# Performance work log

Hardware: AMD Instinct MI355X
Metric: run time of the kernel (lower is better)

Reference implementation:

```python
import jax, jax.numpy as jnp
import numpy as np

N_SRC = 50000
N_DST = 50000
N_EDGE = 600000
HID = 128
NUM_R = 6  # num_ratings + 1 weight matrices


def setup_inputs() -> dict:
    key = jax.random.key(0)
    ks = jax.random.split(key, 8)
    return {
        "src_features": jax.random.normal(ks[0], (N_SRC, HID), dtype=jnp.float32),
        "dst_features": jax.random.normal(ks[1], (N_DST, HID), dtype=jnp.float32),
        "W_r": jax.random.normal(ks[2], (NUM_R, HID, HID), dtype=jnp.float32),
        "W_lin": jax.random.normal(ks[3], (HID, 2 * HID), dtype=jnp.float32) / np.sqrt(2.0 * HID),
        "b_lin": jax.random.normal(ks[4], (HID,), dtype=jnp.float32) * 0.01,
        "edge_src": jax.random.randint(ks[5], (N_EDGE,), 0, N_SRC, dtype=jnp.int32),
        "edge_dst": jax.random.randint(ks[6], (N_EDGE,), 0, N_DST, dtype=jnp.int32),
        "rating": jax.random.randint(ks[7], (N_EDGE,), 0, NUM_R, dtype=jnp.int32),
    }


def reference(src_features, dst_features, W_r, W_lin, b_lin, edge_src, edge_dst, rating):
    # Gather source features per edge: [E, H]
    h_src = src_features[edge_src]
    # Per-edge rating-indexed matvec m_e = W_r[rating_e] @ h_src_e.
    # Avoid materializing [E, H, H] gathered weights: loop over the small
    # fixed set of rating matrices and mask-accumulate dense GEMMs.
    num_r = W_r.shape[0]
    m = jnp.zeros_like(h_src)
    for r in range(num_r):
        m = m + jnp.where((rating == r)[:, None], h_src @ W_r[r].T, jnp.zeros((), h_src.dtype))
    # Mean aggregation into destination nodes (0 for isolated nodes, like DGL).
    num_dst = dst_features.shape[0]
    sums = jax.ops.segment_sum(m, edge_dst, num_segments=num_dst)
    counts = jax.ops.segment_sum(jnp.ones((m.shape[0],), m.dtype), edge_dst, num_segments=num_dst)
    h_neigh = sums / jnp.maximum(counts, 1.0)[:, None]
    # concat + linear + relu
    h_cat = jnp.concatenate([dst_features, h_neigh], axis=1)  # [N_dst, 2H]
    return jax.nn.relu(h_cat @ W_lin.T + b_lin)
```

## Files before the change

kernel.cpp:

```cpp
#include <hip/hip_runtime.h>

#define HID 128
#define BM 64
#define BN 128
#define BKS 32
#define ALD (BKS + 8)
#define SCAN_BLK 256
#define SCAN_ELEMS 1024

typedef float v4f __attribute__((ext_vector_type(4)));
typedef short v8s __attribute__((ext_vector_type(8)));

__device__ __forceinline__ void split_bf16(float v, unsigned short& hi, unsigned short& lo) {
  const unsigned int u = __float_as_uint(v);
  hi = (unsigned short)(u >> 16);
  const float rem = v - __uint_as_float(u & 0xffff0000u);
  lo = (unsigned short)(__float_as_uint(rem) >> 16);
}

__global__ void compose_Bt(const float* __restrict__ W_lin, const float* __restrict__ W_r,
                           unsigned short* __restrict__ Bth, unsigned short* __restrict__ Btl,
                           int KT) {
  const int k = blockIdx.x;
  const int n = threadIdx.x;
  float v;
  if (k < HID) {
    v = W_lin[n * (2 * HID) + k];
  } else {
    const int rr = (k - HID) >> 7;
    const int j  = (k - HID) & (HID - 1);
    const float* wl = W_lin + n * (2 * HID) + HID;
    const float* wr = W_r + (size_t)rr * HID * HID + j;
    float acc = 0.f;
#pragma unroll 8
    for (int i2 = 0; i2 < HID; ++i2)
      acc = fmaf(wl[i2], wr[i2 * HID], acc);
    v = acc;
  }
  unsigned short hi, lo;
  split_bf16(v, hi, lo);
  Bth[(size_t)n * KT + k] = hi;
  Btl[(size_t)n * KT + k] = lo;
}

__global__ void hist_kernel(const int* __restrict__ ed, const int* __restrict__ er,
                            int* __restrict__ hist, int NE, int NUMR) {
  const int i = blockIdx.x * blockDim.x + threadIdx.x;
  if (i < NE) atomicAdd(hist + ed[i] * NUMR + er[i], 1);
}

__global__ __launch_bounds__(SCAN_BLK)
void scan_phaseA(const int* __restrict__ cnt, int* __restrict__ partials, int n) {
  __shared__ int red[SCAN_BLK];
  const int tid = threadIdx.x;
  const int base = blockIdx.x * SCAN_ELEMS + tid * 4;
  int s = 0;
#pragma unroll
  for (int j = 0; j < 4; ++j) {
    const int i = base + j;
    if (i < n) s += cnt[i];
  }
  red[tid] = s;
  __syncthreads();
  for (int off = SCAN_BLK / 2; off > 0; off >>= 1) {
    if (tid < off) red[tid] += red[tid + off];
    __syncthreads();
  }
  if (tid == 0) partials[blockIdx.x] = red[0];
}

__global__ __launch_bounds__(1024)
void scan_phaseB(int* __restrict__ partials, int* __restrict__ offs_n, int nb) {
  __shared__ int ps[1024];
  const int tid = threadIdx.x;
  const int chunk = (nb + 1023) / 1024;
  const int b0 = tid * chunk;
  const int e0 = min(b0 + chunk, nb);
  int s = 0;
  for (int i = b0; i < e0; ++i) s += partials[i];
  ps[tid] = s;
  __syncthreads();
  for (int off = 1; off < 1024; off <<= 1) {
    const int t = (tid >= off) ? ps[tid - off] : 0;
    __syncthreads();
    ps[tid] += t;
    __syncthreads();
  }
  int run = ps[tid] - s;
  for (int i = b0; i < e0; ++i) {
    const int c = partials[i];
    partials[i] = run;
    run += c;
  }
  if (tid == 1023) offs_n[0] = ps[1023];
}

__global__ __launch_bounds__(SCAN_BLK)
void scan_phaseC(const int* __restrict__ cnt, const int* __restrict__ partials,
                 int* __restrict__ offs, int* __restrict__ cursor, int n) {
  __shared__ int tsum[SCAN_BLK];
  const int tid = threadIdx.x;
  const int base = blockIdx.x * SCAN_ELEMS + tid * 4;
  int v[4];
  int s = 0;
#pragma unroll
  for (int j = 0; j < 4; ++j) {
    const int i = base + j;
    v[j] = (i < n) ? cnt[i] : 0;
    s += v[j];
  }
  tsum[tid] = s;
  __syncthreads();
  for (int off = 1; off < SCAN_BLK; off <<= 1) {
    const int t = (tid >= off) ? tsum[tid - off] : 0;
    __syncthreads();
    tsum[tid] += t;
    __syncthreads();
  }
  int run = partials[blockIdx.x] + tsum[tid] - s;
#pragma unroll
  for (int j = 0; j < 4; ++j) {
    const int i = base + j;
    if (i < n) {
      offs[i] = run;
      cursor[i] = run;
      run += v[j];
    }
  }
}

__global__ void reorder_kernel(const int* __restrict__ es, const int* __restrict__ ed,
                               const int* __restrict__ er, int* __restrict__ cursor,
                               int* __restrict__ sorted, int NE, int NUMR) {
  const int i = blockIdx.x * blockDim.x + threadIdx.x;
  if (i < NE) {
    const int key = ed[i] * NUMR + er[i];
    const int pos = atomicAdd(cursor + key, 1);
    sorted[pos] = es[i];
  }
}

__global__ __launch_bounds__(256)
void aggregate_kernel(const float* __restrict__ src, const int* __restrict__ sorted,
                      const int* __restrict__ offs, float* __restrict__ S,
                      int NDST, int NUMR) {
  const int wid = (blockIdx.x * (blockDim.x >> 6)) + (threadIdx.x >> 6);
  const int lane = threadIdx.x & 63;
  if (wid >= NDST * NUMR) return;
  const int d = wid / NUMR;
  const int rloc = wid - d * NUMR;
  const int k = d * NUMR + rloc;
  const int o0 = offs[k], o1 = offs[k + 1];
  const int c0 = offs[d * NUMR], c1 = offs[d * NUMR + NUMR];
  const float inv = 1.0f / fmaxf((float)(c1 - c0), 1.0f);
  float ax = 0.f, ay = 0.f;
  for (int e = o0; e < o1; ++e) {
    const int s = sorted[e];
    const float2 v = *reinterpret_cast<const float2*>(src + (size_t)s * HID + lane * 2);
    ax += v.x; ay += v.y;
  }
  *reinterpret_cast<float2*>(S + (size_t)d * (NUMR * HID) + rloc * HID + lane * 2) =
      make_float2(ax * inv, ay * inv);
}

__global__ __launch_bounds__(256)
void mfma_gemm(const float* __restrict__ dstf, const float* __restrict__ S,
               const unsigned short* __restrict__ Bth, const unsigned short* __restrict__ Btl,
               const float* __restrict__ b_lin, float* __restrict__ out,
               int M, int KT) {
  __shared__ unsigned short Ah[BM][ALD], Al[BM][ALD];
  __shared__ unsigned short Bh[BN][ALD], Bl[BN][ALD];

  const int tid = threadIdx.x;
  const int lane = tid & 63;
  const int wid = tid >> 6;
  const int wm = wid >> 1;
  const int wn = wid & 1;
  const int m0 = blockIdx.x * BM;
  const int l15 = lane & 15;
  const int kq = (lane >> 4) * 8;

  v4f acc[2][4];
#pragma unroll
  for (int i = 0; i < 2; ++i)
#pragma unroll
    for (int j = 0; j < 4; ++j) acc[i][j] = (v4f){0.f, 0.f, 0.f, 0.f};

  const int SSTRIDE = KT - HID;
  const int nkt = KT / BKS;

  for (int kt = 0; kt < nkt; ++kt) {
    const int kg = kt * BKS;
    {
      const int row = tid >> 2;
      const int c8 = (tid & 3) * 8;
      const int rg = m0 + row;
      float4 v0 = make_float4(0.f, 0.f, 0.f, 0.f);
      float4 v1 = make_float4(0.f, 0.f, 0.f, 0.f);
      if (rg < M) {
        const float* srcp = (kg < HID)
            ? dstf + (size_t)rg * HID + kg + c8
            : S + (size_t)rg * SSTRIDE + (kg - HID) + c8;
        v0 = *reinterpret_cast<const float4*>(srcp);
        v1 = *reinterpret_cast<const float4*>(srcp + 4);
      }
      const float vv[8] = {v0.x, v0.y, v0.z, v0.w, v1.x, v1.y, v1.z, v1.w};
      union { v8s v; unsigned short u[8]; } uh, ul;
#pragma unroll
      for (int j = 0; j < 8; ++j) split_bf16(vv[j], uh.u[j], ul.u[j]);
      *reinterpret_cast<v8s*>(&Ah[row][c8]) = uh.v;
      *reinterpret_cast<v8s*>(&Al[row][c8]) = ul.v;
    }
    {
      const int n = tid >> 1;
      const int c16 = (tid & 1) * 16;
      const size_t gb = (size_t)n * KT + kg + c16;
      *reinterpret_cast<v8s*>(&Bh[n][c16]) = *reinterpret_cast<const v8s*>(Bth + gb);
      *reinterpret_cast<v8s*>(&Bh[n][c16 + 8]) = *reinterpret_cast<const v8s*>(Bth + gb + 8);
      *reinterpret_cast<v8s*>(&Bl[n][c16]) = *reinterpret_cast<const v8s*>(Btl + gb);
      *reinterpret_cast<v8s*>(&Bl[n][c16 + 8]) = *reinterpret_cast<const v8s*>(Btl + gb + 8);
    }
    __syncthreads();

    v8s afh[2], afl[2], bfh[4], bfl[4];
#pragma unroll
    for (int fm = 0; fm < 2; ++fm) {
      const int r = wm * 32 + fm * 16 + l15;
      afh[fm] = *reinterpret_cast<const v8s*>(&Ah[r][kq]);
      afl[fm] = *reinterpret_cast<const v8s*>(&Al[r][kq]);
    }
#pragma unroll
    for (int fn = 0; fn < 4; ++fn) {
      const int c = wn * 64 + fn * 16 + l15;
      bfh[fn] = *reinterpret_cast<const v8s*>(&Bh[c][kq]);
      bfl[fn] = *reinterpret_cast<const v8s*>(&Bl[c][kq]);
    }
#pragma unroll
    for (int fm = 0; fm < 2; ++fm)
#pragma unroll
      for (int fn = 0; fn < 4; ++fn) {
        acc[fm][fn] = __builtin_amdgcn_mfma_f32_16x16x32_bf16(afh[fm], bfh[fn], acc[fm][fn], 0, 0, 0);
        acc[fm][fn] = __builtin_amdgcn_mfma_f32_16x16x32_bf16(afh[fm], bfl[fn], acc[fm][fn], 0, 0, 0);
        acc[fm][fn] = __builtin_amdgcn_mfma_f32_16x16x32_bf16(afl[fm], bfh[fn], acc[fm][fn], 0, 0, 0);
      }
    __syncthreads();
  }

#pragma unroll
  for (int fn = 0; fn < 4; ++fn) {
    const int cn = wn * 64 + fn * 16 + l15;
    const float bias = b_lin[cn];
#pragma unroll
    for (int fm = 0; fm < 2; ++fm) {
      const int row0 = m0 + wm * 32 + fm * 16 + (lane >> 4) * 4;
#pragma unroll
      for (int r = 0; r < 4; ++r) {
        const int rg = row0 + r;
        if (rg < M) out[(size_t)rg * HID + cn] = fmaxf(acc[fm][fn][r] + bias, 0.f);
      }
    }
  }
}

extern "C" void kernel_launch(void* const* d_in, const int* in_sizes, int n_in,
                              void* d_out, int out_size, void* d_ws, size_t ws_size,
                              hipStream_t stream) {
  const float* src   = (const float*)d_in[0];
  const float* dstf  = (const float*)d_in[1];
  const float* W_r   = (const float*)d_in[2];
  const float* W_lin = (const float*)d_in[3];
  const float* b_lin = (const float*)d_in[4];
  const int* e_src   = (const int*)d_in[5];
  const int* e_dst   = (const int*)d_in[6];
  const int* e_rat   = (const int*)d_in[7];

  const int N_DST = in_sizes[1] / HID;
  const int NUM_R = in_sizes[2] / (HID * HID);
  const int NE = in_sizes[5];
  const int KT = HID + NUM_R * HID;
  const int NKEY = N_DST * NUM_R;
  const int NB = (NKEY + SCAN_ELEMS - 1) / SCAN_ELEMS;

  const size_t S_b      = (size_t)N_DST * (NUM_R * HID) * sizeof(float);
  const size_t hist_b   = (size_t)NKEY * sizeof(int);
  const size_t offs_b   = (size_t)(NKEY + 1) * sizeof(int);
  const size_t cursor_b = (size_t)NKEY * sizeof(int);
  const size_t sorted_b = (size_t)NE * sizeof(int);
  const size_t part_b   = (size_t)NB * sizeof(int);
  const size_t Bt_b     = (size_t)HID * KT * sizeof(unsigned short);
  const size_t need = S_b + hist_b + offs_b + cursor_b + sorted_b + part_b + 2 * Bt_b + 4096;
  if (ws_size < need) return;

  char* p = (char*)d_ws;
  float* S = (float*)p;            p += (S_b + 255) & ~(size_t)255;
  int* hist = (int*)p;             p += (hist_b + 255) & ~(size_t)255;
  int* offs = (int*)p;             p += (offs_b + 255) & ~(size_t)255;
  int* cursor = (int*)p;           p += (cursor_b + 255) & ~(size_t)255;
  int* sorted = (int*)p;           p += (sorted_b + 255) & ~(size_t)255;
  int* partials = (int*)p;         p += (part_b + 255) & ~(size_t)255;
  unsigned short* Bth = (unsigned short*)p;  p += (Bt_b + 255) & ~(size_t)255;
  unsigned short* Btl = (unsigned short*)p;

  compose_Bt<<<KT, HID, 0, stream>>>(W_lin, W_r, Bth, Btl, KT);
  hipMemsetAsync(hist, 0, hist_b, stream);
  hist_kernel<<<(NE + 255) / 256, 256, 0, stream>>>(e_dst, e_rat, hist, NE, NUM_R);
  scan_phaseA<<<NB, SCAN_BLK, 0, stream>>>(hist, partials, NKEY);
  scan_phaseB<<<1, 1024, 0, stream>>>(partials, offs + NKEY, NB);
  scan_phaseC<<<NB, SCAN_BLK, 0, stream>>>(hist, partials, offs, cursor, NKEY);
  reorder_kernel<<<(NE + 255) / 256, 256, 0, stream>>>(e_src, e_dst, e_rat, cursor,
                                                       sorted, NE, NUM_R);
  const int nwaves = N_DST * NUM_R;
  aggregate_kernel<<<(nwaves + 3) / 4, 256, 0, stream>>>(src, sorted, offs, S,
                                                         N_DST, NUM_R);
  const int mb = (N_DST + BM - 1) / BM;
  mfma_gemm<<<mb, 256, 0, stream>>>(dstf, S, Bth, Btl, b_lin, (float*)d_out,
                                    N_DST, KT);
}
```

Measured before the change: 349.2 us.

## Aggregate per destination node with one wave covering all rating buckets

Replaces the one-wave-per-(dst,rating) aggregation with one wave per destination node. Each half-wave processes alternating edges with float4 loads and accumulates into six per-rating register accumulators chosen by comparing against the bucket boundaries. The two halves are combined with a lane shuffle. This removes the many near-empty waves (about two edges per bucket) and the repeated offset loads, at the cost of more registers and predicated adds per edge.

```diff
diff --git a/kernel.cpp b/kernel.cpp
--- a/kernel.cpp
+++ b/kernel.cpp
@@ -140,6 +140,56 @@
   }
 }
 
+template <int NR>
+__global__ __launch_bounds__(256)
+void aggregate_dst(const float* __restrict__ src, const int* __restrict__ sorted,
+                   const int* __restrict__ offs, float* __restrict__ S, int NDST) {
+  const int d = (blockIdx.x * (blockDim.x >> 6)) + (threadIdx.x >> 6);
+  if (d >= NDST) return;
+  const int lane = threadIdx.x & 63;
+  const int half = lane >> 5;
+  const int c4 = (lane & 31) * 4;
+
+  const int base = d * NR;
+  const int o0 = offs[base];
+  const int oN = offs[base + NR];
+  int bnd[NR - 1];
+#pragma unroll
+  for (int r = 0; r < NR - 1; ++r) bnd[r] = offs[base + 1 + r];
+  const float inv = 1.0f / fmaxf((float)(oN - o0), 1.0f);
+
+  v4f a[NR];
+#pragma unroll
+  for (int r = 0; r < NR; ++r) a[r] = (v4f){0.f, 0.f, 0.f, 0.f};
+
+  for (int e = o0 + half; e < oN; e += 2) {
+    const int s = sorted[e];
+    const v4f v = *reinterpret_cast<const v4f*>(src + (size_t)s * HID + c4);
+    int rloc = 0;
+#pragma unroll
+    for (int r = 0; r < NR - 1; ++r) rloc += (e >= bnd[r]) ? 1 : 0;
+#pragma unroll
+    for (int r = 0; r < NR; ++r) {
+      if (rloc == r) a[r] += v;
+    }
+  }
+
+#pragma unroll
+  for (int r = 0; r < NR; ++r) {
+    v4f t = a[r];
+    v4f o;
+    o[0] = __shfl_xor(t[0], 32);
+    o[1] = __shfl_xor(t[1], 32);
+    o[2] = __shfl_xor(t[2], 32);
+    o[3] = __shfl_xor(t[3], 32);
+    t += o;
+    if (half == 0) {
+      t *= inv;
+      *reinterpret_cast<v4f*>(S + (size_t)d * (NR * HID) + r * HID + c4) = t;
+    }
+  }
+}
+
 __global__ __launch_bounds__(256)
 void aggregate_kernel(const float* __restrict__ src, const int* __restrict__ sorted,
                       const int* __restrict__ offs, float* __restrict__ S,
@@ -309,9 +359,13 @@
   scan_phaseC<<<NB, SCAN_BLK, 0, stream>>>(hist, partials, offs, cursor, NKEY);
   reorder_kernel<<<(NE + 255) / 256, 256, 0, stream>>>(e_src, e_dst, e_rat, cursor,
                                                        sorted, NE, NUM_R);
-  const int nwaves = N_DST * NUM_R;
-  aggregate_kernel<<<(nwaves + 3) / 4, 256, 0, stream>>>(src, sorted, offs, S,
-                                                         N_DST, NUM_R);
+  if (NUM_R == 6) {
+    aggregate_dst<6><<<(N_DST + 3) / 4, 256, 0, stream>>>(src, sorted, offs, S, N_DST);
+  } else {
+    const int nwaves = N_DST * NUM_R;
+    aggregate_kernel<<<(nwaves + 3) / 4, 256, 0, stream>>>(src, sorted, offs, S,
+                                                           N_DST, NUM_R);
+  }
   const int mb = (N_DST + BM - 1) / BM;
   mfma_gemm<<<mb, 256, 0, stream>>>(dstf, S, Bth, Btl, b_lin, (float*)d_out,
                                     N_DST, KT);
```

Measured after the change: 310.2 us. -11.2%, faster.
